# Kernel optimization log

Hardware: AMD Instinct MI355X
Metric: run time of the kernel (lower is better)

## Reference

```python
import jax, jax.numpy as jnp
import numpy as np

LATENT = 40
NUM_FLOWS = 30


def setup_inputs() -> dict:
    key = jax.random.key(0)
    k1, k2, k3, k4 = jax.random.split(key, 4)
    B = 65536
    return {
        "z_k": jax.random.normal(k1, (B, LATENT), dtype=jnp.float32),
        "w": jax.random.normal(k2, (B, NUM_FLOWS * LATENT), dtype=jnp.float32),
        "u": jax.random.normal(k3, (B, NUM_FLOWS * LATENT), dtype=jnp.float32),
        "b": jax.random.normal(k4, (B, NUM_FLOWS), dtype=jnp.float32),
    }


def reference(z_k, w, u, b):
    B = z_k.shape[0]
    # [B, T*L] -> [T, B, L] so lax.scan iterates over flows
    w_s = w.reshape(B, NUM_FLOWS, LATENT).transpose(1, 0, 2)
    u_s = u.reshape(B, NUM_FLOWS, LATENT).transpose(1, 0, 2)
    b_s = b.T[:, :, None]  # [T, B, 1]

    def step(carry, params):
        z, s = carry
        wi, ui, bi = params
        transf = jnp.tanh(jnp.sum(wi * z, axis=1, keepdims=True) + bi)  # [B,1]
        f_z = z + ui * transf
        psi = (1.0 - transf ** 2) * wi  # [B,L]
        ladj = jnp.log(jnp.abs(1.0 + jnp.sum(psi * ui, axis=1, keepdims=True)))
        return (f_z, s + ladj), None

    init = (z_k, jnp.zeros((B, 1), dtype=z_k.dtype))
    (z_out, sum_ladj), _ = jax.lax.scan(step, init, (w_s, u_s, b_s))
    return z_out, sum_ladj
```

## Files before the change

kernel.cpp:

```cpp
#include <hip/hip_runtime.h>

#define LATENT 40
#define NUM_FLOWS 30

__global__ __launch_bounds__(256) void nf_kernel(
    const float* __restrict__ z_k,
    const float* __restrict__ w,
    const float* __restrict__ u,
    const float* __restrict__ bias,
    float* __restrict__ out,
    int B)
{
    int tid  = blockIdx.x * 256 + threadIdx.x;
    int elem = tid >> 3;
    int idx  = tid & 7;
    if (elem >= B) return;
    const bool has_b = (idx < 2);

    const float4* zp = (const float4*)(z_k + (size_t)elem * LATENT);
    float4 zA = zp[idx];
    float4 zB = make_float4(0.f, 0.f, 0.f, 0.f);
    if (has_b) zB = zp[8 + idx];

    const size_t row = (size_t)elem * (NUM_FLOWS * LATENT);
    const float4* wrow = (const float4*)(w + row);
    const float4* urow = (const float4*)(u + row);
    const float* brow = bias + (size_t)elem * NUM_FLOWS;

    float ladj = 0.f;

    #pragma unroll 2
    for (int i = 0; i < NUM_FLOWS; ++i) {
        const float4* wp = wrow + i * 10;
        const float4* up = urow + i * 10;
        float4 wA = wp[idx];
        float4 uA = up[idx];
        float4 wB = make_float4(0.f, 0.f, 0.f, 0.f);
        float4 uB = make_float4(0.f, 0.f, 0.f, 0.f);
        if (has_b) { wB = wp[8 + idx]; uB = up[8 + idx]; }
        float bi = brow[i];

        float s_wz = wA.x * zA.x + wA.y * zA.y + wA.z * zA.z + wA.w * zA.w
                   + wB.x * zB.x + wB.y * zB.y + wB.z * zB.z + wB.w * zB.w;
        float s_wu = wA.x * uA.x + wA.y * uA.y + wA.z * uA.z + wA.w * uA.w
                   + wB.x * uB.x + wB.y * uB.y + wB.z * uB.z + wB.w * uB.w;

        s_wz += __shfl_xor(s_wz, 1); s_wu += __shfl_xor(s_wu, 1);
        s_wz += __shfl_xor(s_wz, 2); s_wu += __shfl_xor(s_wu, 2);
        s_wz += __shfl_xor(s_wz, 4); s_wu += __shfl_xor(s_wu, 4);

        float t = tanhf(s_wz + bi);

        zA.x += uA.x * t; zA.y += uA.y * t; zA.z += uA.z * t; zA.w += uA.w * t;
        zB.x += uB.x * t; zB.y += uB.y * t; zB.z += uB.z * t; zB.w += uB.w * t;

        float det = 1.0f + (1.0f - t * t) * s_wu;
        ladj += logf(fabsf(det));
    }

    float4* zout = (float4*)(out + (size_t)elem * LATENT);
    zout[idx] = zA;
    if (has_b) zout[8 + idx] = zB;
    if (idx == 0) out[(size_t)B * LATENT + elem] = ladj;
}

extern "C" void kernel_launch(void* const* d_in, const int* in_sizes, int n_in,
                              void* d_out, int out_size, void* d_ws, size_t ws_size,
                              hipStream_t stream) {
    const float* z_k  = (const float*)d_in[0];
    const float* w    = (const float*)d_in[1];
    const float* u    = (const float*)d_in[2];
    const float* bias = (const float*)d_in[3];
    float* out = (float*)d_out;

    int B = in_sizes[0] / LATENT;
    int threads = B * 8;
    int block = 256;
    int grid = (threads + block - 1) / block;
    nf_kernel<<<grid, block, 0, stream>>>(z_k, w, u, bias, out, B);
}
```

Before: 622.8 us.

## Prefetch flow params in register ring buffer and rebalance lane element split

Each of the 8 lanes per batch element now holds one float4 plus one scalar, replacing the uneven split where two lanes did an extra float4. This balances loads and removes the has_b branch. A 4-deep register ring buffer prefetches w/u for upcoming flows, and the loop is fully unrolled so loads are issued ahead of the dependent reductions. Bias values are loaded once per lane and injected into the partial sum before the shuffle reduction rather than re-read every flow. The cost is higher register pressure, which may reduce occupancy, and scalar tail loads are only partly coalesced.

```diff
diff --git a/kernel.cpp b/kernel.cpp
--- a/kernel.cpp
+++ b/kernel.cpp
@@ -2,6 +2,7 @@
 
 #define LATENT 40
 #define NUM_FLOWS 30
+#define PF 4
 
 __global__ __launch_bounds__(256) void nf_kernel(
     const float* __restrict__ z_k,
@@ -15,52 +16,77 @@
     int elem = tid >> 3;
     int idx  = tid & 7;
     if (elem >= B) return;
-    const bool has_b = (idx < 2);
 
-    const float4* zp = (const float4*)(z_k + (size_t)elem * LATENT);
-    float4 zA = zp[idx];
-    float4 zB = make_float4(0.f, 0.f, 0.f, 0.f);
-    if (has_b) zB = zp[8 + idx];
+    const float* zrow = z_k + (size_t)elem * LATENT;
+    float4 zA = *(const float4*)(zrow + 4 * idx);
+    float  zt = zrow[32 + idx];
 
-    const size_t row = (size_t)elem * (NUM_FLOWS * LATENT);
-    const float4* wrow = (const float4*)(w + row);
-    const float4* urow = (const float4*)(u + row);
+    const float* wrow = w + (size_t)elem * (NUM_FLOWS * LATENT);
+    const float* urow = u + (size_t)elem * (NUM_FLOWS * LATENT);
+
     const float* brow = bias + (size_t)elem * NUM_FLOWS;
+    float4 bv = make_float4(0.f, 0.f, 0.f, 0.f);
+    {
+        int base = 4 * idx;
+        bv.x = brow[base];
+        bv.y = brow[base + 1];
+        if (base + 2 < NUM_FLOWS) bv.z = brow[base + 2];
+        if (base + 3 < NUM_FLOWS) bv.w = brow[base + 3];
+    }
+
+    float4 wAb[PF], uAb[PF];
+    float  wtb[PF], utb[PF];
+    #pragma unroll
+    for (int i = 0; i < PF; ++i) {
+        const float* wp = wrow + i * LATENT;
+        const float* up = urow + i * LATENT;
+        wAb[i] = *(const float4*)(wp + 4 * idx);
+        wtb[i] = wp[32 + idx];
+        uAb[i] = *(const float4*)(up + 4 * idx);
+        utb[i] = up[32 + idx];
+    }
 
     float ladj = 0.f;
 
-    #pragma unroll 2
+    #pragma unroll
     for (int i = 0; i < NUM_FLOWS; ++i) {
-        const float4* wp = wrow + i * 10;
-        const float4* up = urow + i * 10;
-        float4 wA = wp[idx];
-        float4 uA = up[idx];
-        float4 wB = make_float4(0.f, 0.f, 0.f, 0.f);
-        float4 uB = make_float4(0.f, 0.f, 0.f, 0.f);
-        if (has_b) { wB = wp[8 + idx]; uB = up[8 + idx]; }
-        float bi = brow[i];
+        const int s = i % PF;
+        float4 wA = wAb[s];  float wt = wtb[s];
+        float4 uA = uAb[s];  float ut = utb[s];
 
-        float s_wz = wA.x * zA.x + wA.y * zA.y + wA.z * zA.z + wA.w * zA.w
-                   + wB.x * zB.x + wB.y * zB.y + wB.z * zB.z + wB.w * zB.w;
-        float s_wu = wA.x * uA.x + wA.y * uA.y + wA.z * uA.z + wA.w * uA.w
-                   + wB.x * uB.x + wB.y * uB.y + wB.z * uB.z + wB.w * uB.w;
+        if (i + PF < NUM_FLOWS) {
+            const float* wp = wrow + (i + PF) * LATENT;
+            const float* up = urow + (i + PF) * LATENT;
+            wAb[s] = *(const float4*)(wp + 4 * idx);
+            wtb[s] = wp[32 + idx];
+            uAb[s] = *(const float4*)(up + 4 * idx);
+            utb[s] = up[32 + idx];
+        }
+
+        float s_wz = wA.x * zA.x + wA.y * zA.y + wA.z * zA.z + wA.w * zA.w + wt * zt;
+        float s_wu = wA.x * uA.x + wA.y * uA.y + wA.z * uA.z + wA.w * uA.w + wt * ut;
+
+        if (idx == (i >> 2)) {
+            const int c = i & 3;
+            s_wz += (c == 0) ? bv.x : (c == 1) ? bv.y : (c == 2) ? bv.z : bv.w;
+        }
 
         s_wz += __shfl_xor(s_wz, 1); s_wu += __shfl_xor(s_wu, 1);
         s_wz += __shfl_xor(s_wz, 2); s_wu += __shfl_xor(s_wu, 2);
         s_wz += __shfl_xor(s_wz, 4); s_wu += __shfl_xor(s_wu, 4);
 
-        float t = tanhf(s_wz + bi);
+        float t = tanhf(s_wz);
 
         zA.x += uA.x * t; zA.y += uA.y * t; zA.z += uA.z * t; zA.w += uA.w * t;
-        zB.x += uB.x * t; zB.y += uB.y * t; zB.z += uB.z * t; zB.w += uB.w * t;
+        zt   += ut * t;
 
-        float det = 1.0f + (1.0f - t * t) * s_wu;
+        float det = fmaf(1.0f - t * t, s_wu, 1.0f);
         ladj += logf(fabsf(det));
     }
 
-    float4* zout = (float4*)(out + (size_t)elem * LATENT);
-    zout[idx] = zA;
-    if (has_b) zout[8 + idx] = zB;
+    float* zout = out + (size_t)elem * LATENT;
+    *(float4*)(zout + 4 * idx) = zA;
+    zout[32 + idx] = zt;
     if (idx == 0) out[(size_t)B * LATENT + elem] = ladj;
 }
 
```

Measured after the change: 608.0 us. 2.4% less time.
